# Performance work log

Measured on AMD Instinct MI355X. Metric: run time of the kernel, lower is better.

Reference implementation:

```python
import jax, jax.numpy as jnp
import numpy as np

N_NODES = 50000
N_EDGES = 800000
N_GRAPHS = 64
IN_DIM, HID, MLP_HID, NUM_CLASSES = 384, 128, 64, 1


def setup_inputs() -> dict:
    key = jax.random.key(0)
    ks = jax.random.split(key, 10)
    x = jax.random.normal(ks[0], (N_NODES, IN_DIM), jnp.float32)
    edge_index = jax.random.randint(ks[1], (2, N_EDGES), 0, N_NODES, dtype=jnp.int32)
    batch = jnp.sort(jax.random.randint(ks[2], (N_NODES,), 0, N_GRAPHS, dtype=jnp.int32))

    def glorot(k, shape):
        fan_in = shape[0]
        return jax.random.normal(k, shape, jnp.float32) / jnp.sqrt(jnp.float32(fan_in))

    return {
        "x": x,
        "edge_index": edge_index,
        "batch": batch,
        "W1": glorot(ks[3], (IN_DIM, HID)),  "b1": jnp.zeros((HID,), jnp.float32),
        "W2": glorot(ks[4], (HID, HID)),     "b2": jnp.zeros((HID,), jnp.float32),
        "W3": glorot(ks[5], (HID, HID)),     "b3": jnp.zeros((HID,), jnp.float32),
        "Wm1": glorot(ks[6], (HID, MLP_HID)), "bm1": jnp.zeros((MLP_HID,), jnp.float32),
        "Wm2": glorot(ks[7], (MLP_HID, NUM_CLASSES)), "bm2": jnp.zeros((NUM_CLASSES,), jnp.float32),
    }


def _gcn_conv(x, W, b, src, dst, dis):
    # PyG GCNConv: h = x W; aggregate D^-1/2 (A+I) D^-1/2 h; add bias.
    n = x.shape[0]
    h = x @ W                               # [N, out]
    enorm = dis[src] * dis[dst]             # [E] symmetric normalization
    msgs = h[src] * enorm[:, None]          # gather + scale
    agg = jax.ops.segment_sum(msgs, dst, num_segments=n)
    agg = agg + h * (dis * dis)[:, None]    # self-loop contribution
    return agg + b


def reference(x, edge_index, batch, W1, b1, W2, b2, W3, b3, Wm1, bm1, Wm2, bm2):
    src, dst = edge_index[0], edge_index[1]
    n = x.shape[0]
    # degree over A + I (self-loops added, as in PyG gcn_norm)
    deg = jax.ops.segment_sum(jnp.ones((src.shape[0],), x.dtype), dst, num_segments=n) + 1.0
    dis = jax.lax.rsqrt(deg)

    h = jax.nn.relu(_gcn_conv(x, W1, b1, src, dst, dis))
    h = jax.nn.relu(_gcn_conv(h, W2, b2, src, dst, dis))
    h = jax.nn.relu(_gcn_conv(h, W3, b3, src, dst, dis))

    # global mean pool over graphs
    counts = jax.ops.segment_sum(jnp.ones((n,), x.dtype), batch, num_segments=N_GRAPHS)
    pooled = jax.ops.segment_sum(h, batch, num_segments=N_GRAPHS)
    pooled = pooled / jnp.maximum(counts, 1.0)[:, None]   # [G, HID]

    # MLP head (dropout = identity in eval mode)
    z = jax.nn.relu(pooled @ Wm1 + bm1)
    out = z @ Wm2 + bm2                                    # [G, 1]
    return out
```

## Files before the change

kernel.cpp:

```cpp
#include <hip/hip_runtime.h>
#include <hip/hip_bf16.h>

#define N_NODES 50000
#define N_EDGES 800000
#define N_GRAPHS 64
#define IN_DIM 384
#define HID 128
#define MLP_HID 64

#define SCAN_BLOCKS ((N_NODES + 255) / 256)
#define GEMM_BLOCKS ((N_NODES + 127) / 128)
#define GATHER_BLOCKS (N_NODES / 4)

typedef __attribute__((ext_vector_type(8))) short short8;
typedef __attribute__((ext_vector_type(4))) float f32x4;
typedef unsigned int u32;

__global__ __launch_bounds__(256) void count_kernel(const int* __restrict__ dst,
                                                    int* __restrict__ cnt, int E) {
    int t = blockIdx.x * 256 + threadIdx.x;
    if (t < E) atomicAdd(&cnt[dst[t]], 1);
}

__global__ __launch_bounds__(256) void bsum_kernel(const int* __restrict__ cnt,
                                                   int* __restrict__ bsum) {
    __shared__ int sh[256];
    const int t = threadIdx.x;
    const int i = blockIdx.x * 256 + t;
    sh[t] = (i < N_NODES) ? cnt[i] : 0;
    __syncthreads();
#pragma unroll
    for (int off = 128; off > 0; off >>= 1) {
        if (t < off) sh[t] += sh[t + off];
        __syncthreads();
    }
    if (t == 0) bsum[blockIdx.x] = sh[0];
}

__global__ __launch_bounds__(256) void bscan_kernel(const int* __restrict__ bsum,
                                                    int* __restrict__ boff,
                                                    int* __restrict__ rowptr) {
    __shared__ int sh[256];
    const int t = threadIdx.x;
    int v = (t < SCAN_BLOCKS) ? bsum[t] : 0;
    sh[t] = v;
    __syncthreads();
#pragma unroll
    for (int off = 1; off < 256; off <<= 1) {
        int u = 0;
        if (t >= off) u = sh[t - off];
        __syncthreads();
        if (t >= off) sh[t] += u;
        __syncthreads();
    }
    if (t < SCAN_BLOCKS) boff[t] = sh[t] - v;
    if (t == 255) rowptr[N_NODES] = sh[255];
}

__global__ __launch_bounds__(256) void final_scan_kernel(const int* __restrict__ cnt,
                                                         const int* __restrict__ boff,
                                                         int* __restrict__ rowptr,
                                                         int* __restrict__ cursor,
                                                         float* __restrict__ dis) {
    __shared__ int sh[256];
    const int t = threadIdx.x;
    const int i = blockIdx.x * 256 + t;
    const int c = (i < N_NODES) ? cnt[i] : 0;
    sh[t] = c;
    __syncthreads();
#pragma unroll
    for (int off = 1; off < 256; off <<= 1) {
        int u = 0;
        if (t >= off) u = sh[t - off];
        __syncthreads();
        if (t >= off) sh[t] += u;
        __syncthreads();
    }
    if (i < N_NODES) {
        const int pos = boff[blockIdx.x] + sh[t] - c;
        rowptr[i] = pos;
        cursor[i] = pos;
        dis[i] = rsqrtf((float)c + 1.0f);
    }
}

__global__ __launch_bounds__(256) void fill_kernel(const int* __restrict__ ei,
                                                   int* __restrict__ cursor,
                                                   int* __restrict__ csr, int E) {
    int e = blockIdx.x * 256 + threadIdx.x;
    if (e >= E) return;
    int s = ei[e];
    int d = ei[E + e];
    int pos = atomicAdd(&cursor[d], 1);
    csr[pos] = s;
}

__device__ __forceinline__ void wsplit_one(const float* W, ushort* hi, ushort* lo,
                                           int K, int t) {
    const int k = t >> 7;
    const int c = t & 127;
    const float f = W[t];
    const u32 u = __float_as_uint(f);
    const u32 h = u & 0xFFFF0000u;
    const float lf = f - __uint_as_float(h);
    hi[c * K + k] = (ushort)(u >> 16);
    lo[c * K + k] = (ushort)(__float_as_uint(lf) >> 16);
}

__global__ __launch_bounds__(256) void wsplit_kernel(const float* __restrict__ W1,
                                                     const float* __restrict__ W2,
                                                     const float* __restrict__ W3,
                                                     ushort* __restrict__ w1hi, ushort* __restrict__ w1lo,
                                                     ushort* __restrict__ w2hi, ushort* __restrict__ w2lo,
                                                     ushort* __restrict__ w3hi, ushort* __restrict__ w3lo) {
    int t = blockIdx.x * 256 + threadIdx.x;
    if (t < IN_DIM * HID) wsplit_one(W1, w1hi, w1lo, IN_DIM, t);
    if (t < HID * HID) {
        wsplit_one(W2, w2hi, w2lo, HID, t);
        wsplit_one(W3, w3hi, w3lo, HID, t);
    }
}

template <int K, bool RELU_IN>
__global__ __launch_bounds__(256) void gemm_mfma_kernel(const float* __restrict__ X,
                                                        const ushort* __restrict__ Wthi,
                                                        const ushort* __restrict__ Wtlo,
                                                        const float* __restrict__ dis,
                                                        float* __restrict__ Hs, int M) {
    __shared__ ushort Ahi[128][40];
    __shared__ ushort Alo[128][40];
    __shared__ ushort Bhi[128][40];
    __shared__ ushort Blo[128][40];

    const int tid = threadIdx.x;
    const int row0 = blockIdx.x * 128;

    const int srow = tid >> 1;
    const int skq  = (tid & 1) << 4;

    const int lane = tid & 63;
    const int wave = tid >> 6;
    const int wr = (wave >> 1) * 64;
    const int wc = (wave & 1) * 64;
    const int li = lane & 15;
    const int kb = (lane >> 4) << 3;

    f32x4 acc[4][4];
#pragma unroll
    for (int m = 0; m < 4; ++m)
#pragma unroll
        for (int n = 0; n < 4; ++n) acc[m][n] = (f32x4){0.f, 0.f, 0.f, 0.f};

    for (int k0 = 0; k0 < K; k0 += 32) {
        {
            const int gr = row0 + srow;
            const float* src = &X[(size_t)(gr < M ? gr : (M - 1)) * K + k0 + skq];
            float f[16];
            *reinterpret_cast<float4*>(f)      = *reinterpret_cast<const float4*>(src);
            *reinterpret_cast<float4*>(f + 4)  = *reinterpret_cast<const float4*>(src + 4);
            *reinterpret_cast<float4*>(f + 8)  = *reinterpret_cast<const float4*>(src + 8);
            *reinterpret_cast<float4*>(f + 12) = *reinterpret_cast<const float4*>(src + 12);
            u32 hp[8], lp[8];
#pragma unroll
            for (int i = 0; i < 8; ++i) {
                float f0 = f[2 * i], f1 = f[2 * i + 1];
                if (RELU_IN) { f0 = fmaxf(f0, 0.f); f1 = fmaxf(f1, 0.f); }
                const u32 u0 = __float_as_uint(f0), u1 = __float_as_uint(f1);
                const u32 h0 = u0 & 0xFFFF0000u, h1 = u1 & 0xFFFF0000u;
                const float l0 = f0 - __uint_as_float(h0);
                const float l1 = f1 - __uint_as_float(h1);
                hp[i] = (h0 >> 16) | h1;
                lp[i] = (__float_as_uint(l0) >> 16) | (__float_as_uint(l1) & 0xFFFF0000u);
            }
            u32* dh = (u32*)&Ahi[srow][skq];
            u32* dl = (u32*)&Alo[srow][skq];
            *reinterpret_cast<uint4*>(dh)     = make_uint4(hp[0], hp[1], hp[2], hp[3]);
            *reinterpret_cast<uint4*>(dh + 4) = make_uint4(hp[4], hp[5], hp[6], hp[7]);
            *reinterpret_cast<uint4*>(dl)     = make_uint4(lp[0], lp[1], lp[2], lp[3]);
            *reinterpret_cast<uint4*>(dl + 4) = make_uint4(lp[4], lp[5], lp[6], lp[7]);
        }
        {
            const ushort* sh = &Wthi[srow * K + k0 + skq];
            const ushort* sl = &Wtlo[srow * K + k0 + skq];
            *reinterpret_cast<uint4*>(&Bhi[srow][skq])     = *reinterpret_cast<const uint4*>(sh);
            *reinterpret_cast<uint4*>(&Bhi[srow][skq + 8]) = *reinterpret_cast<const uint4*>(sh + 8);
            *reinterpret_cast<uint4*>(&Blo[srow][skq])     = *reinterpret_cast<const uint4*>(sl);
            *reinterpret_cast<uint4*>(&Blo[srow][skq + 8]) = *reinterpret_cast<const uint4*>(sl + 8);
        }
        __syncthreads();
        short8 ah[4], al[4];
#pragma unroll
        for (int m = 0; m < 4; ++m) {
            ah[m] = *reinterpret_cast<const short8*>(&Ahi[wr + m * 16 + li][kb]);
            al[m] = *reinterpret_cast<const short8*>(&Alo[wr + m * 16 + li][kb]);
        }
#pragma unroll
        for (int n = 0; n < 4; ++n) {
            const short8 bh = *reinterpret_cast<const short8*>(&Bhi[wc + n * 16 + li][kb]);
            const short8 bl = *reinterpret_cast<const short8*>(&Blo[wc + n * 16 + li][kb]);
#pragma unroll
            for (int m = 0; m < 4; ++m) {
                acc[m][n] = __builtin_amdgcn_mfma_f32_16x16x32_bf16(ah[m], bh, acc[m][n], 0, 0, 0);
                acc[m][n] = __builtin_amdgcn_mfma_f32_16x16x32_bf16(ah[m], bl, acc[m][n], 0, 0, 0);
                acc[m][n] = __builtin_amdgcn_mfma_f32_16x16x32_bf16(al[m], bh, acc[m][n], 0, 0, 0);
            }
        }
        __syncthreads();
    }
    const int rbase = (lane >> 4) << 2;
#pragma unroll
    for (int m = 0; m < 4; ++m) {
        const int gr0 = row0 + wr + m * 16 + rbase;
#pragma unroll
        for (int r = 0; r < 4; ++r) {
            const int grow = gr0 + r;
            if (grow < M) {
                const float dv = dis[grow];
#pragma unroll
                for (int n = 0; n < 4; ++n) {
                    Hs[(size_t)grow * 128 + wc + n * 16 + li] = acc[m][n][r] * dv;
                }
            }
        }
    }
}

template <bool POOL>
__global__ __launch_bounds__(256) void gather_kernel(const int* __restrict__ rowptr,
                                                     const int* __restrict__ csr,
                                                     const float* __restrict__ Hs,
                                                     const float* __restrict__ dis,
                                                     const float* __restrict__ b,
                                                     float* __restrict__ AGG,
                                                     const int* __restrict__ batch,
                                                     float* __restrict__ pooled) {
    const int wave = threadIdx.x >> 6;
    const int lane = threadIdx.x & 63;
    const int node = blockIdx.x * 4 + wave;
    const int f2 = lane * 2;
    const int beg = rowptr[node];
    const int end = rowptr[node + 1];

    float2 acc = *reinterpret_cast<const float2*>(&Hs[(size_t)node * 128 + f2]);
    int i = beg;
    for (; i + 4 <= end; i += 4) {
        const int s0 = csr[i], s1 = csr[i + 1], s2 = csr[i + 2], s3 = csr[i + 3];
        const float2 v0 = *reinterpret_cast<const float2*>(&Hs[(size_t)s0 * 128 + f2]);
        const float2 v1 = *reinterpret_cast<const float2*>(&Hs[(size_t)s1 * 128 + f2]);
        const float2 v2 = *reinterpret_cast<const float2*>(&Hs[(size_t)s2 * 128 + f2]);
        const float2 v3 = *reinterpret_cast<const float2*>(&Hs[(size_t)s3 * 128 + f2]);
        acc.x += (v0.x + v1.x) + (v2.x + v3.x);
        acc.y += (v0.y + v1.y) + (v2.y + v3.y);
    }
    for (; i < end; ++i) {
        const int s = csr[i];
        const float2 v = *reinterpret_cast<const float2*>(&Hs[(size_t)s * 128 + f2]);
        acc.x += v.x;
        acc.y += v.y;
    }
    const float d = dis[node];
    float2 o;
    o.x = fmaf(acc.x, d, b[f2]);
    o.y = fmaf(acc.y, d, b[f2 + 1]);

    if (!POOL) {
        *reinterpret_cast<float2*>(&AGG[(size_t)node * 128 + f2]) = o;
    } else {
        o.x = fmaxf(o.x, 0.f);
        o.y = fmaxf(o.y, 0.f);
        __shared__ float part[4][128];
        __shared__ int gs[4];
        const int g = batch[node];
        if (lane == 0) gs[wave] = g;
        part[wave][f2] = o.x;
        part[wave][f2 + 1] = o.y;
        __syncthreads();
        if (gs[0] == gs[1] && gs[1] == gs[2] && gs[2] == gs[3]) {
            if (threadIdx.x < 128) {
                const float s = (part[0][threadIdx.x] + part[1][threadIdx.x]) +
                                (part[2][threadIdx.x] + part[3][threadIdx.x]);
                atomicAdd(&pooled[gs[0] * HID + threadIdx.x], s);
            }
        } else {
            atomicAdd(&pooled[g * HID + f2], o.x);
            atomicAdd(&pooled[g * HID + f2 + 1], o.y);
        }
    }
}

__global__ __launch_bounds__(128) void pooldiv_kernel(const int* __restrict__ batch,
                                                      float* __restrict__ pooled, int n) {
    const int g = blockIdx.x;
    int lo = 0, hi = n;
    while (lo < hi) { int mid = (lo + hi) >> 1; if (batch[mid] < g) lo = mid + 1; else hi = mid; }
    const int start = lo;
    hi = n;
    while (lo < hi) { int mid = (lo + hi) >> 1; if (batch[mid] < g + 1) lo = mid + 1; else hi = mid; }
    const float cnt = (float)(lo - start);
    pooled[g * HID + threadIdx.x] /= fmaxf(cnt, 1.f);
}

__global__ __launch_bounds__(256) void mlp_kernel(const float* __restrict__ pooled,
                                                  const float* __restrict__ Wm1,
                                                  const float* __restrict__ bm1,
                                                  const float* __restrict__ Wm2,
                                                  const float* __restrict__ bm2,
                                                  float* __restrict__ out) {
    __shared__ float P[N_GRAPHS][HID];
    __shared__ float Wl[HID][MLP_HID];
    const int tid = threadIdx.x;
    for (int i = tid; i < N_GRAPHS * HID; i += 256) P[i >> 7][i & 127] = pooled[i];
    for (int i = tid; i < HID * MLP_HID; i += 256) Wl[i >> 6][i & 63] = Wm1[i];
    __syncthreads();
    const int g = tid >> 2;
    const int jb = tid & 3;
    float part = 0.f;
#pragma unroll
    for (int jj = 0; jj < 16; ++jj) {
        const int j = jb * 16 + jj;
        float z = bm1[j];
        for (int k = 0; k < HID; ++k) z = fmaf(P[g][k], Wl[k][j], z);
        z = fmaxf(z, 0.f);
        part = fmaf(z, Wm2[j], part);
    }
    part += __shfl_xor(part, 1);
    part += __shfl_xor(part, 2);
    if (jb == 0) out[g] = part + bm2[0];
}

extern "C" void kernel_launch(void* const* d_in, const int* in_sizes, int n_in,
                              void* d_out, int out_size, void* d_ws, size_t ws_size,
                              hipStream_t stream) {
    const float* x   = (const float*)d_in[0];
    const int*   ei  = (const int*)d_in[1];
    const int*   bat = (const int*)d_in[2];
    const float* W1  = (const float*)d_in[3];
    const float* b1  = (const float*)d_in[4];
    const float* W2  = (const float*)d_in[5];
    const float* b2  = (const float*)d_in[6];
    const float* W3  = (const float*)d_in[7];
    const float* b3  = (const float*)d_in[8];
    const float* Wm1 = (const float*)d_in[9];
    const float* bm1 = (const float*)d_in[10];
    const float* Wm2 = (const float*)d_in[11];
    const float* bm2 = (const float*)d_in[12];
    float* out = (float*)d_out;

    int*   cnt    = (int*)d_ws;
    int*   cursor = cnt + 50048;
    int*   rowptr = cursor + 50048;
    int*   csr    = rowptr + 50056;
    int*   bsum   = csr + 800000;
    int*   boff   = bsum + 256;
    float* dis    = (float*)(boff + 256);
    float* H      = dis + 50048;
    float* AGG    = H + N_NODES * HID;
    float* pooled = AGG + N_NODES * HID;
    ushort* wt1hi = (ushort*)(pooled + 8192);
    ushort* wt1lo = wt1hi + IN_DIM * HID;
    ushort* wt2hi = wt1lo + IN_DIM * HID;
    ushort* wt2lo = wt2hi + HID * HID;
    ushort* wt3hi = wt2lo + HID * HID;
    ushort* wt3lo = wt3hi + HID * HID;

    hipMemsetAsync(cnt, 0, N_NODES * sizeof(int), stream);
    hipMemsetAsync(pooled, 0, N_GRAPHS * HID * sizeof(float), stream);

    count_kernel<<<(N_EDGES + 255) / 256, 256, 0, stream>>>(ei + N_EDGES, cnt, N_EDGES);
    bsum_kernel<<<SCAN_BLOCKS, 256, 0, stream>>>(cnt, bsum);
    bscan_kernel<<<1, 256, 0, stream>>>(bsum, boff, rowptr);
    final_scan_kernel<<<SCAN_BLOCKS, 256, 0, stream>>>(cnt, boff, rowptr, cursor, dis);
    fill_kernel<<<(N_EDGES + 255) / 256, 256, 0, stream>>>(ei, cursor, csr, N_EDGES);

    wsplit_kernel<<<(IN_DIM * HID + 255) / 256, 256, 0, stream>>>(
        W1, W2, W3, wt1hi, wt1lo, wt2hi, wt2lo, wt3hi, wt3lo);

    gemm_mfma_kernel<IN_DIM, false><<<GEMM_BLOCKS, 256, 0, stream>>>(x, wt1hi, wt1lo, dis, H, N_NODES);
    gather_kernel<false><<<GATHER_BLOCKS, 256, 0, stream>>>(rowptr, csr, H, dis, b1, AGG, bat, pooled);
    gemm_mfma_kernel<HID, true><<<GEMM_BLOCKS, 256, 0, stream>>>(AGG, wt2hi, wt2lo, dis, H, N_NODES);
    gather_kernel<false><<<GATHER_BLOCKS, 256, 0, stream>>>(rowptr, csr, H, dis, b2, AGG, bat, pooled);
    gemm_mfma_kernel<HID, true><<<GEMM_BLOCKS, 256, 0, stream>>>(AGG, wt3hi, wt3lo, dis, H, N_NODES);
    gather_kernel<true><<<GATHER_BLOCKS, 256, 0, stream>>>(rowptr, csr, H, dis, b3, AGG, bat, pooled);

    pooldiv_kernel<<<N_GRAPHS, 128, 0, stream>>>(bat, pooled, N_NODES);
    mlp_kernel<<<1, 256, 0, stream>>>(pooled, Wm1, bm1, Wm2, bm2, out);
}
```

Measured before the change: 522.8 us.

## Bucket CSR edges by source range and gather in source-bucket order for L2 locality

Builds the CSR with 16 source-range buckets per destination node, so each node's neighbours are grouped by source index block. Each gather wave now handles 8 destination nodes and walks all of them through bucket 0, then bucket 1, and so on, so concurrent reads of H fall into the same source slice and should reuse L2/cache better. The pooling epilogue now reduces 32 rows per block with run-length grouping by graph. In exchange, the segment array is 16x larger (memset, scans, counts), and the per-bucket inner loops are short and serial, which lowers memory-level parallelism per wave.

```diff
diff --git a/kernel.cpp b/kernel.cpp
--- a/kernel.cpp
+++ b/kernel.cpp
@@ -8,26 +8,39 @@
 #define HID 128
 #define MLP_HID 64
 
-#define SCAN_BLOCKS ((N_NODES + 255) / 256)
+#define NB 16
+#define BSH 12
+#define NTOT (N_NODES * NB)
+#define BS2_BLOCKS ((NTOT + 1023) / 1024)
 #define GEMM_BLOCKS ((N_NODES + 127) / 128)
-#define GATHER_BLOCKS (N_NODES / 4)
+#define GATH_BLOCKS ((N_NODES + 31) / 32)
 
 typedef __attribute__((ext_vector_type(8))) short short8;
 typedef __attribute__((ext_vector_type(4))) float f32x4;
 typedef unsigned int u32;
 
-__global__ __launch_bounds__(256) void count_kernel(const int* __restrict__ dst,
-                                                    int* __restrict__ cnt, int E) {
+__global__ __launch_bounds__(256) void count2_kernel(const int* __restrict__ ei,
+                                                     int* __restrict__ seg, int E) {
     int t = blockIdx.x * 256 + threadIdx.x;
-    if (t < E) atomicAdd(&cnt[dst[t]], 1);
-}
-
-__global__ __launch_bounds__(256) void bsum_kernel(const int* __restrict__ cnt,
-                                                   int* __restrict__ bsum) {
+    if (t < E) {
+        const int s = ei[t];
+        const int d = ei[E + t];
+        atomicAdd(&seg[d * NB + (s >> BSH)], 1);
+    }
+}
+
+__global__ __launch_bounds__(256) void bsum2_kernel(const int* __restrict__ seg,
+                                                    int* __restrict__ bsum) {
     __shared__ int sh[256];
     const int t = threadIdx.x;
-    const int i = blockIdx.x * 256 + t;
-    sh[t] = (i < N_NODES) ? cnt[i] : 0;
+    const int i0 = blockIdx.x * 1024 + t * 4;
+    int s = 0;
+#pragma unroll
+    for (int k = 0; k < 4; ++k) {
+        const int i = i0 + k;
+        if (i < NTOT) s += seg[i];
+    }
+    sh[t] = s;
     __syncthreads();
 #pragma unroll
     for (int off = 128; off > 0; off >>= 1) {
@@ -37,15 +50,20 @@
     if (t == 0) bsum[blockIdx.x] = sh[0];
 }
 
-__global__ __launch_bounds__(256) void bscan_kernel(const int* __restrict__ bsum,
-                                                    int* __restrict__ boff,
-                                                    int* __restrict__ rowptr) {
+__global__ __launch_bounds__(256) void bscan2_kernel(const int* __restrict__ bsum,
+                                                     int* __restrict__ boff) {
     __shared__ int sh[256];
     const int t = threadIdx.x;
-    int v = (t < SCAN_BLOCKS) ? bsum[t] : 0;
-    sh[t] = v;
+    int v[4];
+    int s = 0;
+#pragma unroll
+    for (int k = 0; k < 4; ++k) {
+        const int i = t * 4 + k;
+        v[k] = (i < BS2_BLOCKS) ? bsum[i] : 0;
+        s += v[k];
+    }
+    sh[t] = s;
     __syncthreads();
-#pragma unroll
     for (int off = 1; off < 256; off <<= 1) {
         int u = 0;
         if (t >= off) u = sh[t - off];
@@ -53,22 +71,30 @@
         if (t >= off) sh[t] += u;
         __syncthreads();
     }
-    if (t < SCAN_BLOCKS) boff[t] = sh[t] - v;
-    if (t == 255) rowptr[N_NODES] = sh[255];
-}
-
-__global__ __launch_bounds__(256) void final_scan_kernel(const int* __restrict__ cnt,
-                                                         const int* __restrict__ boff,
-                                                         int* __restrict__ rowptr,
-                                                         int* __restrict__ cursor,
-                                                         float* __restrict__ dis) {
+    int base = sh[t] - s;
+#pragma unroll
+    for (int k = 0; k < 4; ++k) {
+        const int i = t * 4 + k;
+        if (i < BS2_BLOCKS) boff[i] = base;
+        base += v[k];
+    }
+}
+
+__global__ __launch_bounds__(256) void final2_kernel(int* __restrict__ seg,
+                                                     const int* __restrict__ boff) {
     __shared__ int sh[256];
     const int t = threadIdx.x;
-    const int i = blockIdx.x * 256 + t;
-    const int c = (i < N_NODES) ? cnt[i] : 0;
-    sh[t] = c;
+    const int i0 = blockIdx.x * 1024 + t * 4;
+    int c[4];
+    int s = 0;
+#pragma unroll
+    for (int k = 0; k < 4; ++k) {
+        const int i = i0 + k;
+        c[k] = (i < NTOT) ? seg[i] : 0;
+        s += c[k];
+    }
+    sh[t] = s;
     __syncthreads();
-#pragma unroll
     for (int off = 1; off < 256; off <<= 1) {
         int u = 0;
         if (t >= off) u = sh[t - off];
@@ -76,22 +102,33 @@
         if (t >= off) sh[t] += u;
         __syncthreads();
     }
-    if (i < N_NODES) {
-        const int pos = boff[blockIdx.x] + sh[t] - c;
-        rowptr[i] = pos;
-        cursor[i] = pos;
-        dis[i] = rsqrtf((float)c + 1.0f);
-    }
-}
-
-__global__ __launch_bounds__(256) void fill_kernel(const int* __restrict__ ei,
-                                                   int* __restrict__ cursor,
-                                                   int* __restrict__ csr, int E) {
+    int run = boff[blockIdx.x] + sh[t] - s;
+#pragma unroll
+    for (int k = 0; k < 4; ++k) {
+        const int i = i0 + k;
+        if (i < NTOT) seg[i] = run;
+        run += c[k];
+    }
+}
+
+__global__ __launch_bounds__(256) void dis2_kernel(const int* __restrict__ seg,
+                                                   float* __restrict__ dis) {
+    const int d = blockIdx.x * 256 + threadIdx.x;
+    if (d < N_NODES) {
+        const int start = seg[d * NB];
+        const int next = (d == N_NODES - 1) ? N_EDGES : seg[(d + 1) * NB];
+        dis[d] = rsqrtf((float)(next - start) + 1.0f);
+    }
+}
+
+__global__ __launch_bounds__(256) void fill2_kernel(const int* __restrict__ ei,
+                                                    int* __restrict__ seg,
+                                                    int* __restrict__ csr, int E) {
     int e = blockIdx.x * 256 + threadIdx.x;
     if (e >= E) return;
-    int s = ei[e];
-    int d = ei[E + e];
-    int pos = atomicAdd(&cursor[d], 1);
+    const int s = ei[e];
+    const int d = ei[E + e];
+    const int pos = atomicAdd(&seg[d * NB + (s >> BSH)], 1);
     csr[pos] = s;
 }
 
@@ -226,64 +263,92 @@
 }
 
 template <bool POOL>
-__global__ __launch_bounds__(256) void gather_kernel(const int* __restrict__ rowptr,
-                                                     const int* __restrict__ csr,
-                                                     const float* __restrict__ Hs,
-                                                     const float* __restrict__ dis,
-                                                     const float* __restrict__ b,
-                                                     float* __restrict__ AGG,
-                                                     const int* __restrict__ batch,
-                                                     float* __restrict__ pooled) {
+__global__ __launch_bounds__(256) void gather2_kernel(const int* __restrict__ seg,
+                                                      const int* __restrict__ csr,
+                                                      const float* __restrict__ Hs,
+                                                      const float* __restrict__ dis,
+                                                      const float* __restrict__ bias,
+                                                      float* __restrict__ AGG,
+                                                      const int* __restrict__ batch,
+                                                      float* __restrict__ pooled) {
     const int wave = threadIdx.x >> 6;
     const int lane = threadIdx.x & 63;
-    const int node = blockIdx.x * 4 + wave;
-    const int f2 = lane * 2;
-    const int beg = rowptr[node];
-    const int end = rowptr[node + 1];
-
-    float2 acc = *reinterpret_cast<const float2*>(&Hs[(size_t)node * 128 + f2]);
-    int i = beg;
-    for (; i + 4 <= end; i += 4) {
-        const int s0 = csr[i], s1 = csr[i + 1], s2 = csr[i + 2], s3 = csr[i + 3];
-        const float2 v0 = *reinterpret_cast<const float2*>(&Hs[(size_t)s0 * 128 + f2]);
-        const float2 v1 = *reinterpret_cast<const float2*>(&Hs[(size_t)s1 * 128 + f2]);
-        const float2 v2 = *reinterpret_cast<const float2*>(&Hs[(size_t)s2 * 128 + f2]);
-        const float2 v3 = *reinterpret_cast<const float2*>(&Hs[(size_t)s3 * 128 + f2]);
-        acc.x += (v0.x + v1.x) + (v2.x + v3.x);
-        acc.y += (v0.y + v1.y) + (v2.y + v3.y);
-    }
-    for (; i < end; ++i) {
-        const int s = csr[i];
-        const float2 v = *reinterpret_cast<const float2*>(&Hs[(size_t)s * 128 + f2]);
-        acc.x += v.x;
-        acc.y += v.y;
-    }
-    const float d = dis[node];
-    float2 o;
-    o.x = fmaf(acc.x, d, b[f2]);
-    o.y = fmaf(acc.y, d, b[f2 + 1]);
+    const int dBlk = blockIdx.x * 32;
+    const int d0 = dBlk + wave * 8;
+    const int f = lane * 2;
+    int nrows = N_NODES - d0;
+    nrows = nrows < 0 ? 0 : (nrows > 8 ? 8 : nrows);
+
+    float2 acc[8];
+    int pc[8];
+#pragma unroll
+    for (int r = 0; r < 8; ++r) {
+        if (r < nrows) {
+            const int d = d0 + r;
+            acc[r] = *reinterpret_cast<const float2*>(&Hs[(size_t)d * 128 + f]);
+            pc[r] = (d == 0) ? 0 : seg[d * NB - 1];
+        } else {
+            acc[r] = make_float2(0.f, 0.f);
+            pc[r] = 0;
+        }
+    }
+
+    for (int b = 0; b < NB; ++b) {
+#pragma unroll
+        for (int r = 0; r < 8; ++r) {
+            if (r >= nrows) break;
+            const int p1 = seg[(d0 + r) * NB + b];
+            for (int e = pc[r]; e < p1; ++e) {
+                const int s = csr[e];
+                const float2 v = *reinterpret_cast<const float2*>(&Hs[(size_t)s * 128 + f]);
+                acc[r].x += v.x;
+                acc[r].y += v.y;
+            }
+            pc[r] = p1;
+        }
+    }
 
     if (!POOL) {
-        *reinterpret_cast<float2*>(&AGG[(size_t)node * 128 + f2]) = o;
+#pragma unroll
+        for (int r = 0; r < 8; ++r) {
+            if (r >= nrows) break;
+            const int d = d0 + r;
+            const float dv = dis[d];
+            float2 o;
+            o.x = fmaf(acc[r].x, dv, bias[f]);
+            o.y = fmaf(acc[r].y, dv, bias[f + 1]);
+            *reinterpret_cast<float2*>(&AGG[(size_t)d * 128 + f]) = o;
+        }
     } else {
-        o.x = fmaxf(o.x, 0.f);
-        o.y = fmaxf(o.y, 0.f);
-        __shared__ float part[4][128];
-        __shared__ int gs[4];
-        const int g = batch[node];
-        if (lane == 0) gs[wave] = g;
-        part[wave][f2] = o.x;
-        part[wave][f2 + 1] = o.y;
-        __syncthreads();
-        if (gs[0] == gs[1] && gs[1] == gs[2] && gs[2] == gs[3]) {
-            if (threadIdx.x < 128) {
-                const float s = (part[0][threadIdx.x] + part[1][threadIdx.x]) +
-                                (part[2][threadIdx.x] + part[3][threadIdx.x]);
-                atomicAdd(&pooled[gs[0] * HID + threadIdx.x], s);
-            }
-        } else {
-            atomicAdd(&pooled[g * HID + f2], o.x);
-            atomicAdd(&pooled[g * HID + f2 + 1], o.y);
+        __shared__ float part[32][128];
+#pragma unroll
+        for (int r = 0; r < 8; ++r) {
+            float2 o = make_float2(0.f, 0.f);
+            if (r < nrows) {
+                const float dv = dis[d0 + r];
+                o.x = fmaxf(fmaf(acc[r].x, dv, bias[f]), 0.f);
+                o.y = fmaxf(fmaf(acc[r].y, dv, bias[f + 1]), 0.f);
+            }
+            part[wave * 8 + r][f] = o.x;
+            part[wave * 8 + r][f + 1] = o.y;
+        }
+        __syncthreads();
+        if (threadIdx.x < 128) {
+            const int fq = threadIdx.x;
+            float s = 0.f;
+            int gcur = -1;
+            for (int r = 0; r < 32; ++r) {
+                const int d = dBlk + r;
+                if (d >= N_NODES) break;
+                const int g = batch[d];
+                if (g != gcur) {
+                    if (gcur >= 0) atomicAdd(&pooled[gcur * HID + fq], s);
+                    gcur = g;
+                    s = 0.f;
+                }
+                s += part[r][fq];
+            }
+            if (gcur >= 0) atomicAdd(&pooled[gcur * HID + fq], s);
         }
     }
 }
@@ -346,15 +411,13 @@
     const float* bm2 = (const float*)d_in[12];
     float* out = (float*)d_out;
 
-    int*   cnt    = (int*)d_ws;
-    int*   cursor = cnt + 50048;
-    int*   rowptr = cursor + 50048;
-    int*   csr    = rowptr + 50056;
-    int*   bsum   = csr + 800000;
-    int*   boff   = bsum + 256;
-    float* dis    = (float*)(boff + 256);
-    float* H      = dis + 50048;
-    float* AGG    = H + N_NODES * HID;
+    int*   seg    = (int*)d_ws;
+    int*   csr    = seg + NTOT;
+    int*   bsum2  = csr + 800000;
+    int*   boff2  = bsum2 + 1024;
+    float* dis    = (float*)(boff2 + 1024);
+    float* Hs     = dis + 50048;
+    float* AGG    = Hs + N_NODES * HID;
     float* pooled = AGG + N_NODES * HID;
     ushort* wt1hi = (ushort*)(pooled + 8192);
     ushort* wt1lo = wt1hi + IN_DIM * HID;
@@ -363,24 +426,25 @@
     ushort* wt3hi = wt2lo + HID * HID;
     ushort* wt3lo = wt3hi + HID * HID;
 
-    hipMemsetAsync(cnt, 0, N_NODES * sizeof(int), stream);
+    hipMemsetAsync(seg, 0, NTOT * sizeof(int), stream);
     hipMemsetAsync(pooled, 0, N_GRAPHS * HID * sizeof(float), stream);
 
-    count_kernel<<<(N_EDGES + 255) / 256, 256, 0, stream>>>(ei + N_EDGES, cnt, N_EDGES);
-    bsum_kernel<<<SCAN_BLOCKS, 256, 0, stream>>>(cnt, bsum);
-    bscan_kernel<<<1, 256, 0, stream>>>(bsum, boff, rowptr);
-    final_scan_kernel<<<SCAN_BLOCKS, 256, 0, stream>>>(cnt, boff, rowptr, cursor, dis);
-    fill_kernel<<<(N_EDGES + 255) / 256, 256, 0, stream>>>(ei, cursor, csr, N_EDGES);
+    count2_kernel<<<(N_EDGES + 255) / 256, 256, 0, stream>>>(ei, seg, N_EDGES);
+    bsum2_kernel<<<BS2_BLOCKS, 256, 0, stream>>>(seg, bsum2);
+    bscan2_kernel<<<1, 256, 0, stream>>>(bsum2, boff2);
+    final2_kernel<<<BS2_BLOCKS, 256, 0, stream>>>(seg, boff2);
+    dis2_kernel<<<(N_NODES + 255) / 256, 256, 0, stream>>>(seg, dis);
+    fill2_kernel<<<(N_EDGES + 255) / 256, 256, 0, stream>>>(ei, seg, csr, N_EDGES);
 
     wsplit_kernel<<<(IN_DIM * HID + 255) / 256, 256, 0, stream>>>(
         W1, W2, W3, wt1hi, wt1lo, wt2hi, wt2lo, wt3hi, wt3lo);
 
-    gemm_mfma_kernel<IN_DIM, false><<<GEMM_BLOCKS, 256, 0, stream>>>(x, wt1hi, wt1lo, dis, H, N_NODES);
-    gather_kernel<false><<<GATHER_BLOCKS, 256, 0, stream>>>(rowptr, csr, H, dis, b1, AGG, bat, pooled);
-    gemm_mfma_kernel<HID, true><<<GEMM_BLOCKS, 256, 0, stream>>>(AGG, wt2hi, wt2lo, dis, H, N_NODES);
-    gather_kernel<false><<<GATHER_BLOCKS, 256, 0, stream>>>(rowptr, csr, H, dis, b2, AGG, bat, pooled);
-    gemm_mfma_kernel<HID, true><<<GEMM_BLOCKS, 256, 0, stream>>>(AGG, wt3hi, wt3lo, dis, H, N_NODES);
-    gather_kernel<true><<<GATHER_BLOCKS, 256, 0, stream>>>(rowptr, csr, H, dis, b3, AGG, bat, pooled);
+    gemm_mfma_kernel<IN_DIM, false><<<GEMM_BLOCKS, 256, 0, stream>>>(x, wt1hi, wt1lo, dis, Hs, N_NODES);
+    gather2_kernel<false><<<GATH_BLOCKS, 256, 0, stream>>>(seg, csr, Hs, dis, b1, AGG, bat, pooled);
+    gemm_mfma_kernel<HID, true><<<GEMM_BLOCKS, 256, 0, stream>>>(AGG, wt2hi, wt2lo, dis, Hs, N_NODES);
+    gather2_kernel<false><<<GATH_BLOCKS, 256, 0, stream>>>(seg, csr, Hs, dis, b2, AGG, bat, pooled);
+    gemm_mfma_kernel<HID, true><<<GEMM_BLOCKS, 256, 0, stream>>>(AGG, wt3hi, wt3lo, dis, Hs, N_NODES);
+    gather2_kernel<true><<<GATH_BLOCKS, 256, 0, stream>>>(seg, csr, Hs, dis, b3, AGG, bat, pooled);
 
     pooldiv_kernel<<<N_GRAPHS, 128, 0, stream>>>(bat, pooled, N_NODES);
     mlp_kernel<<<1, 256, 0, stream>>>(pooled, Wm1, bm1, Wm2, bm2, out);
```

Result: slower. 663.3 us (+26.9%).
